# Optimization experiments

Measured on AMD Instinct MI355X. Metric: run time of the kernel, lower is better.

## Reference

```python
import jax, jax.numpy as jnp
import numpy as np

B = 8192
I = 1024  # input_size
H = 1024  # hidden_size


def setup_inputs() -> dict:
    key = jax.random.key(0)
    ks = jax.random.split(key, 8)
    s_i = 1.0 / np.sqrt(I)
    s_h = 1.0 / np.sqrt(H)
    return {
        "x": jax.random.normal(ks[0], (B, I), dtype=jnp.float32),
        "h": jax.random.normal(ks[1], (B, H), dtype=jnp.float32),
        # nn.Linear weights have shape [out, in]; y = x @ W.T
        "W_wz": jax.random.uniform(ks[2], (H, I), jnp.float32, -s_i, s_i),
        "W_uz": jax.random.uniform(ks[3], (H, H), jnp.float32, -s_h, s_h),
        "W_wr": jax.random.uniform(ks[4], (H, I), jnp.float32, -s_i, s_i),
        "W_ur": jax.random.uniform(ks[5], (H, H), jnp.float32, -s_h, s_h),
        "W_u": jax.random.uniform(ks[6], (H, H), jnp.float32, -s_h, s_h),
        "W_w": jax.random.uniform(ks[7], (H, I), jnp.float32, -s_i, s_i),
    }


def reference(x, h, W_wz, W_uz, W_wr, W_ur, W_u, W_w):
    # Fuse the three x-projections and the two h-projections into grouped GEMMs.
    # [B, 3H] = x @ [I, 3H]
    xp = x @ jnp.concatenate([W_wz, W_wr, W_w], axis=0).T
    hp = h @ jnp.concatenate([W_uz, W_ur], axis=0).T  # [B, 2H]
    z = jax.nn.sigmoid(xp[:, :H] + hp[:, :H])
    r = jax.nn.sigmoid(xp[:, H:2 * H] + hp[:, H:])
    h_t = jnp.tanh((r * h) @ W_u.T + xp[:, 2 * H:])
    return z * h + (1.0 - z) * h_t
```

## Files before the change

kernel.cpp:

```cpp
#include <hip/hip_runtime.h>

typedef unsigned short u16;
typedef __attribute__((ext_vector_type(8))) short bf16x8;
typedef __attribute__((ext_vector_type(4))) float f32x4;

__device__ __forceinline__ u16 f2b(float f) {
  unsigned u = __float_as_uint(f);
  u += 0x7FFFu + ((u >> 16) & 1u);
  return (u16)(u >> 16);
}
__device__ __forceinline__ float sigm(float x) { return 1.0f / (1.0f + __expf(-x)); }
__device__ __forceinline__ float tanh_f(float x) { return 1.0f - 2.0f / (__expf(2.0f * x) + 1.0f); }

__device__ __forceinline__ void cp16(const u16* g, u16* l) {
  __builtin_amdgcn_global_load_lds(
      (const __attribute__((address_space(1))) unsigned int*)g,
      (__attribute__((address_space(3))) unsigned int*)l, 16, 0, 0);
}

__global__ __launch_bounds__(256) void pack_xh(const float* __restrict__ x,
                                               const float* __restrict__ h,
                                               u16* __restrict__ xhb) {
  int idx = blockIdx.x * 256 + threadIdx.x;
  int row = idx >> 9;
  int k = (idx & 511) << 2;
  const float* src = (k < 1024) ? (x + row * 1024 + k) : (h + row * 1024 + (k - 1024));
  float4 v = *reinterpret_cast<const float4*>(src);
  ushort4 o = make_ushort4(f2b(v.x), f2b(v.y), f2b(v.z), f2b(v.w));
  *reinterpret_cast<ushort4*>(xhb + ((size_t)idx << 2)) = o;
}

__global__ __launch_bounds__(256) void pack_w1(const float* __restrict__ Wwz,
                                               const float* __restrict__ Wuz,
                                               const float* __restrict__ Wwr,
                                               const float* __restrict__ Wur,
                                               const float* __restrict__ Ww,
                                               u16* __restrict__ W1b) {
  int idx = blockIdx.x * 256 + threadIdx.x;
  int n = idx >> 9;
  int k = (idx & 511) << 2;
  float4 v = make_float4(0.f, 0.f, 0.f, 0.f);
  if (n < 1024) {
    v = (k < 1024) ? *reinterpret_cast<const float4*>(Wwz + n * 1024 + k)
                   : *reinterpret_cast<const float4*>(Wuz + n * 1024 + (k - 1024));
  } else if (n < 2048) {
    int nn = n - 1024;
    v = (k < 1024) ? *reinterpret_cast<const float4*>(Wwr + nn * 1024 + k)
                   : *reinterpret_cast<const float4*>(Wur + nn * 1024 + (k - 1024));
  } else {
    int nn = n - 2048;
    if (k < 1024) v = *reinterpret_cast<const float4*>(Ww + nn * 1024 + k);
  }
  ushort4 o = make_ushort4(f2b(v.x), f2b(v.y), f2b(v.z), f2b(v.w));
  *reinterpret_cast<ushort4*>(W1b + ((size_t)idx << 2)) = o;
}

__global__ __launch_bounds__(256) void pack_wu(const float* __restrict__ Wu,
                                               u16* __restrict__ Wub) {
  int idx = blockIdx.x * 256 + threadIdx.x;
  float4 v = *reinterpret_cast<const float4*>(Wu + ((size_t)idx << 2));
  ushort4 o = make_ushort4(f2b(v.x), f2b(v.y), f2b(v.z), f2b(v.w));
  *reinterpret_cast<ushort4*>(Wub + ((size_t)idx << 2)) = o;
}

__device__ __forceinline__ void gemm_core(const u16* __restrict__ A, const u16* __restrict__ Bm,
                                          int lda, int ldb, int m0, int n0, int ksteps,
                                          u16* a_lds, u16* b_lds, f32x4 acc[4][4]) {
  const int tid = threadIdx.x;
  const int lane = tid & 63;
  const int wave = tid >> 6;
  const int wr = wave >> 1, wc = wave & 1;
  const int srow = tid >> 2;
  const int scol = (tid & 3) << 3;
  const u16* ga = A + (size_t)(m0 + srow) * lda + scol;
  const u16* gb = Bm + (size_t)(n0 + srow) * ldb + scol;
  u16* la = a_lds + tid * 8;
  u16* lb = b_lds + tid * 8;
  const int fr = lane & 15;
  const int fk = (lane >> 4) << 3;

  for (int kt = 0; kt < ksteps; ++kt) {
    const int k0 = kt * 32;
    cp16(ga + k0, la);
    cp16(ga + (size_t)64 * lda + k0, la + 64 * 32);
    cp16(gb + k0, lb);
    cp16(gb + (size_t)64 * ldb + k0, lb + 64 * 32);
    __syncthreads();

    bf16x8 af[4], bfr[4];
#pragma unroll
    for (int m = 0; m < 4; ++m)
      af[m] = *reinterpret_cast<const bf16x8*>(&a_lds[(wr * 64 + m * 16 + fr) * 32 + fk]);
#pragma unroll
    for (int n = 0; n < 4; ++n)
      bfr[n] = *reinterpret_cast<const bf16x8*>(&b_lds[(wc * 64 + n * 16 + fr) * 32 + fk]);
#pragma unroll
    for (int m = 0; m < 4; ++m)
#pragma unroll
      for (int n = 0; n < 4; ++n)
        acc[m][n] = __builtin_amdgcn_mfma_f32_16x16x32_bf16(af[m], bfr[n], acc[m][n], 0, 0, 0);
    __syncthreads();
  }
}

__global__ __launch_bounds__(256) void gemm1_k(const u16* __restrict__ xhb,
                                               const u16* __restrict__ W1b,
                                               const float* __restrict__ h,
                                               float* __restrict__ zout,
                                               u16* __restrict__ rhb,
                                               float* __restrict__ xwb) {
  __shared__ u16 a_lds[128 * 32];
  __shared__ u16 b_lds[128 * 32];
  const int m0 = blockIdx.y * 128;
  const int n0 = blockIdx.x * 128;
  const int ksteps = (n0 >= 2048) ? 32 : 64;
  f32x4 acc[4][4];
#pragma unroll
  for (int m = 0; m < 4; ++m)
#pragma unroll
    for (int n = 0; n < 4; ++n) acc[m][n] = (f32x4){0.f, 0.f, 0.f, 0.f};

  gemm_core(xhb, W1b, 2048, 2048, m0, n0, ksteps, a_lds, b_lds, acc);

  const int lane = threadIdx.x & 63;
  const int wave = threadIdx.x >> 6;
  const int wr = wave >> 1, wc = wave & 1;
  const int rbase = m0 + wr * 64 + ((lane >> 4) << 2);
  const int cbase = n0 + wc * 64 + (lane & 15);
  const int region = n0 >> 10;
#pragma unroll
  for (int m = 0; m < 4; ++m) {
#pragma unroll
    for (int n = 0; n < 4; ++n) {
      const int col = cbase + n * 16;
#pragma unroll
      for (int j = 0; j < 4; ++j) {
        const int row = rbase + m * 16 + j;
        const float v = acc[m][n][j];
        if (region == 0) {
          zout[(size_t)row * 1024 + col] = sigm(v);
        } else if (region == 1) {
          const size_t idx = (size_t)row * 1024 + (col - 1024);
          rhb[idx] = f2b(sigm(v) * h[idx]);
        } else {
          xwb[(size_t)row * 1024 + (col - 2048)] = v;
        }
      }
    }
  }
}

__global__ __launch_bounds__(256) void gemm2_k(const u16* __restrict__ rhb,
                                               const u16* __restrict__ Wub,
                                               const float* __restrict__ h,
                                               const float* __restrict__ xwb,
                                               float* __restrict__ out) {
  __shared__ u16 a_lds[128 * 32];
  __shared__ u16 b_lds[128 * 32];
  const int m0 = blockIdx.y * 128;
  const int n0 = blockIdx.x * 128;
  f32x4 acc[4][4];
#pragma unroll
  for (int m = 0; m < 4; ++m)
#pragma unroll
    for (int n = 0; n < 4; ++n) acc[m][n] = (f32x4){0.f, 0.f, 0.f, 0.f};

  gemm_core(rhb, Wub, 1024, 1024, m0, n0, 32, a_lds, b_lds, acc);

  const int lane = threadIdx.x & 63;
  const int wave = threadIdx.x >> 6;
  const int wr = wave >> 1, wc = wave & 1;
  const int rbase = m0 + wr * 64 + ((lane >> 4) << 2);
  const int cbase = n0 + wc * 64 + (lane & 15);
#pragma unroll
  for (int m = 0; m < 4; ++m) {
#pragma unroll
    for (int n = 0; n < 4; ++n) {
      const int col = cbase + n * 16;
#pragma unroll
      for (int j = 0; j < 4; ++j) {
        const int row = rbase + m * 16 + j;
        const size_t idx = (size_t)row * 1024 + col;
        const float z = out[idx];
        const float hv = h[idx];
        const float ht = tanh_f(acc[m][n][j] + xwb[idx]);
        out[idx] = z * hv + (1.0f - z) * ht;
      }
    }
  }
}

extern "C" void kernel_launch(void* const* d_in, const int* in_sizes, int n_in,
                              void* d_out, int out_size, void* d_ws, size_t ws_size,
                              hipStream_t stream) {
  const float* x   = (const float*)d_in[0];
  const float* h   = (const float*)d_in[1];
  const float* Wwz = (const float*)d_in[2];
  const float* Wuz = (const float*)d_in[3];
  const float* Wwr = (const float*)d_in[4];
  const float* Wur = (const float*)d_in[5];
  const float* Wu  = (const float*)d_in[6];
  const float* Ww  = (const float*)d_in[7];
  float* out = (float*)d_out;

  char* ws = (char*)d_ws;
  u16*   xhb = (u16*)(ws);
  u16*   W1b = (u16*)(ws + 33554432);
  u16*   Wub = (u16*)(ws + 46137344);
  u16*   rhb = (u16*)(ws + 48234496);
  float* xwb = (float*)(ws + 65011712);

  pack_xh<<<16384, 256, 0, stream>>>(x, h, xhb);
  pack_w1<<<6144, 256, 0, stream>>>(Wwz, Wuz, Wwr, Wur, Ww, W1b);
  pack_wu<<<1024, 256, 0, stream>>>(Wu, Wub);
  gemm1_k<<<dim3(24, 64), 256, 0, stream>>>(xhb, W1b, h, out, rhb, xwb);
  gemm2_k<<<dim3(8, 64), 256, 0, stream>>>(rhb, Wub, h, xwb, out);
}
```

Measured before the change: 340.9 us.

## Rewrite GEMM core with 256x256 tiles, double-buffered async LDS and swizzle

Replaces the 128x128 single-buffered GEMM core with a 256x256 tile, 8-wave kernel that uses a K-tile of 64, double-buffered LDS filled by direct global-to-LDS loads, and an XOR swizzle to avoid bank conflicts. Prefetch of the next A tile and the tile after next for B is interleaved with MFMA quarters, using explicit waitcnt, barriers and priority hints. The aim is to hide global load latency, cut per-k-step barrier overhead and raise data reuse per block. In exchange it uses more registers and LDS per block and launches fewer blocks, 384 for the first GEMM and 128 for the second, which may leave CUs underused on the second GEMM.

```diff
diff --git a/kernel.cpp b/kernel.cpp
--- a/kernel.cpp
+++ b/kernel.cpp
@@ -63,80 +63,121 @@
   *reinterpret_cast<ushort4*>(Wub + ((size_t)idx << 2)) = o;
 }
 
-__device__ __forceinline__ void gemm_core(const u16* __restrict__ A, const u16* __restrict__ Bm,
-                                          int lda, int ldb, int m0, int n0, int ksteps,
-                                          u16* a_lds, u16* b_lds, f32x4 acc[4][4]) {
+__device__ __forceinline__ void core8(const u16* __restrict__ Ag, const u16* __restrict__ Bg,
+                                      int lda, int ldb, int NT,
+                                      u16* a_lds, u16* b_lds, f32x4 acc[8][4]) {
   const int tid = threadIdx.x;
   const int lane = tid & 63;
-  const int wave = tid >> 6;
-  const int wr = wave >> 1, wc = wave & 1;
-  const int srow = tid >> 2;
-  const int scol = (tid & 3) << 3;
-  const u16* ga = A + (size_t)(m0 + srow) * lda + scol;
-  const u16* gb = Bm + (size_t)(n0 + srow) * ldb + scol;
-  u16* la = a_lds + tid * 8;
-  u16* lb = b_lds + tid * 8;
-  const int fr = lane & 15;
-  const int fk = (lane >> 4) << 3;
-
-  for (int kt = 0; kt < ksteps; ++kt) {
-    const int k0 = kt * 32;
-    cp16(ga + k0, la);
-    cp16(ga + (size_t)64 * lda + k0, la + 64 * 32);
-    cp16(gb + k0, lb);
-    cp16(gb + (size_t)64 * ldb + k0, lb + 64 * 32);
-    __syncthreads();
-
-    bf16x8 af[4], bfr[4];
-#pragma unroll
-    for (int m = 0; m < 4; ++m)
-      af[m] = *reinterpret_cast<const bf16x8*>(&a_lds[(wr * 64 + m * 16 + fr) * 32 + fk]);
-#pragma unroll
-    for (int n = 0; n < 4; ++n)
-      bfr[n] = *reinterpret_cast<const bf16x8*>(&b_lds[(wc * 64 + n * 16 + fr) * 32 + fk]);
-#pragma unroll
-    for (int m = 0; m < 4; ++m)
-#pragma unroll
-      for (int n = 0; n < 4; ++n)
-        acc[m][n] = __builtin_amdgcn_mfma_f32_16x16x32_bf16(af[m], bfr[n], acc[m][n], 0, 0, 0);
-    __syncthreads();
-  }
-}
-
-__global__ __launch_bounds__(256) void gemm1_k(const u16* __restrict__ xhb,
-                                               const u16* __restrict__ W1b,
-                                               const float* __restrict__ h,
-                                               float* __restrict__ zout,
-                                               u16* __restrict__ rhb,
-                                               float* __restrict__ xwb) {
-  __shared__ u16 a_lds[128 * 32];
-  __shared__ u16 b_lds[128 * 32];
-  const int m0 = blockIdx.y * 128;
-  const int n0 = blockIdx.x * 128;
-  const int ksteps = (n0 >= 2048) ? 32 : 64;
-  f32x4 acc[4][4];
-#pragma unroll
-  for (int m = 0; m < 4; ++m)
+  const int wid = tid >> 6;
+  const int wr = wid >> 2;
+  const int wc = wid & 3;
+
+  const int plo = tid * 16;
+  const int olo = plo ^ (((plo >> 9) & 1) << 5);
+  const int r0 = olo >> 7;
+  const int c2 = olo & 127;
+
+  const int arl = (((lane & 15) * 128) + (((lane >> 4) * 16) ^ (((lane >> 2) & 1) << 5))) >> 1;
+
+  auto stageA = [&](int h, int tg, int tb) {
+    const u16* g = Ag + (size_t)(h * 128 + r0) * lda + (c2 >> 1) + (size_t)tg * 64;
+    u16* l = a_lds + tb * 16384 + h * 8192 + tid * 8;
+    cp16(g, l);
+    cp16(g + (size_t)64 * lda, l + 4096);
+  };
+  auto stageB = [&](int h, int tg, int tb) {
+    const u16* g = Bg + (size_t)(h * 128 + r0) * ldb + (c2 >> 1) + (size_t)tg * 64;
+    u16* l = b_lds + tb * 16384 + h * 8192 + tid * 8;
+    cp16(g, l);
+    cp16(g + (size_t)64 * ldb, l + 4096);
+  };
+
+  stageA(0, 0, 0); stageA(1, 0, 0);
+  stageB(0, 0, 0); stageB(1, 0, 0);
+  stageB(0, 1, 1); stageB(1, 1, 1);
+  asm volatile("s_waitcnt vmcnt(4)" ::: "memory");
+  __builtin_amdgcn_s_barrier();
+  __builtin_amdgcn_sched_barrier(0);
+
+  for (int t = 0; t < NT; ++t) {
+    const int buf = t & 1;
+    const int abase = buf * 16384 + wr * 8192;
+    const int bbase = buf * 16384 + (wc >> 1) * 8192 + (wc & 1) * 4096;
+    bf16x8 bfr[4][2];
+#pragma unroll
+    for (int q = 0; q < 4; ++q) {
+      bf16x8 af[2][2];
+#pragma unroll
+      for (int m = 0; m < 2; ++m)
+#pragma unroll
+        for (int ks = 0; ks < 2; ++ks)
+          af[m][ks] = *reinterpret_cast<const bf16x8*>(
+              a_lds + abase + (q * 2 + m) * 1024 + ks * 32 + arl);
+      if (q == 0) {
+#pragma unroll
+        for (int nf = 0; nf < 4; ++nf)
+#pragma unroll
+          for (int ks = 0; ks < 2; ++ks)
+            bfr[nf][ks] = *reinterpret_cast<const bf16x8*>(
+                b_lds + bbase + nf * 1024 + ks * 32 + arl);
+      }
+      if (q == 0)      { if (t + 1 < NT) stageA(0, t + 1, (t + 1) & 1); }
+      else if (q == 1) { if (t + 1 < NT) stageA(1, t + 1, (t + 1) & 1); }
+      else if (q == 2) { if (t + 2 < NT) stageB(0, t + 2, buf); }
+      else             { if (t + 2 < NT) stageB(1, t + 2, buf);
+                         asm volatile("s_waitcnt vmcnt(4)" ::: "memory"); }
+      __builtin_amdgcn_s_barrier();
+      __builtin_amdgcn_sched_barrier(0);
+      __builtin_amdgcn_s_setprio(1);
+#pragma unroll
+      for (int m = 0; m < 2; ++m)
+#pragma unroll
+        for (int nf = 0; nf < 4; ++nf)
+#pragma unroll
+          for (int ks = 0; ks < 2; ++ks)
+            acc[q * 2 + m][nf] = __builtin_amdgcn_mfma_f32_16x16x32_bf16(
+                af[m][ks], bfr[nf][ks], acc[q * 2 + m][nf], 0, 0, 0);
+      __builtin_amdgcn_s_setprio(0);
+      __builtin_amdgcn_s_barrier();
+      __builtin_amdgcn_sched_barrier(0);
+    }
+  }
+}
+
+__global__ __launch_bounds__(512, 2) void gemm1_k(const u16* __restrict__ xhb,
+                                                  const u16* __restrict__ W1b,
+                                                  const float* __restrict__ h,
+                                                  float* __restrict__ zout,
+                                                  u16* __restrict__ rhb,
+                                                  float* __restrict__ xwb) {
+  __shared__ u16 a_lds[32768];
+  __shared__ u16 b_lds[32768];
+  const int m0 = blockIdx.y * 256;
+  const int n0 = blockIdx.x * 256;
+  const int NT = (n0 >= 2048) ? 16 : 32;
+  f32x4 acc[8][4];
+#pragma unroll
+  for (int m = 0; m < 8; ++m)
 #pragma unroll
     for (int n = 0; n < 4; ++n) acc[m][n] = (f32x4){0.f, 0.f, 0.f, 0.f};
 
-  gemm_core(xhb, W1b, 2048, 2048, m0, n0, ksteps, a_lds, b_lds, acc);
+  core8(xhb + (size_t)m0 * 2048, W1b + (size_t)n0 * 2048, 2048, 2048, NT, a_lds, b_lds, acc);
 
   const int lane = threadIdx.x & 63;
-  const int wave = threadIdx.x >> 6;
-  const int wr = wave >> 1, wc = wave & 1;
-  const int rbase = m0 + wr * 64 + ((lane >> 4) << 2);
+  const int wid = threadIdx.x >> 6;
+  const int wr = wid >> 2, wc = wid & 3;
+  const int rbase = m0 + wr * 128 + ((lane >> 4) << 2);
   const int cbase = n0 + wc * 64 + (lane & 15);
   const int region = n0 >> 10;
 #pragma unroll
-  for (int m = 0; m < 4; ++m) {
-#pragma unroll
-    for (int n = 0; n < 4; ++n) {
-      const int col = cbase + n * 16;
+  for (int mq = 0; mq < 8; ++mq) {
+#pragma unroll
+    for (int nf = 0; nf < 4; ++nf) {
+      const int col = cbase + nf * 16;
 #pragma unroll
       for (int j = 0; j < 4; ++j) {
-        const int row = rbase + m * 16 + j;
-        const float v = acc[m][n][j];
+        const int row = rbase + mq * 16 + j;
+        const float v = acc[mq][nf][j];
         if (region == 0) {
           zout[(size_t)row * 1024 + col] = sigm(v);
         } else if (region == 1) {
@@ -150,40 +191,40 @@
   }
 }
 
-__global__ __launch_bounds__(256) void gemm2_k(const u16* __restrict__ rhb,
-                                               const u16* __restrict__ Wub,
-                                               const float* __restrict__ h,
-                                               const float* __restrict__ xwb,
-                                               float* __restrict__ out) {
-  __shared__ u16 a_lds[128 * 32];
-  __shared__ u16 b_lds[128 * 32];
-  const int m0 = blockIdx.y * 128;
-  const int n0 = blockIdx.x * 128;
-  f32x4 acc[4][4];
-#pragma unroll
-  for (int m = 0; m < 4; ++m)
+__global__ __launch_bounds__(512, 2) void gemm2_k(const u16* __restrict__ rhb,
+                                                  const u16* __restrict__ Wub,
+                                                  const float* __restrict__ h,
+                                                  const float* __restrict__ xwb,
+                                                  float* __restrict__ out) {
+  __shared__ u16 a_lds[32768];
+  __shared__ u16 b_lds[32768];
+  const int m0 = blockIdx.y * 256;
+  const int n0 = blockIdx.x * 256;
+  f32x4 acc[8][4];
+#pragma unroll
+  for (int m = 0; m < 8; ++m)
 #pragma unroll
     for (int n = 0; n < 4; ++n) acc[m][n] = (f32x4){0.f, 0.f, 0.f, 0.f};
 
-  gemm_core(rhb, Wub, 1024, 1024, m0, n0, 32, a_lds, b_lds, acc);
+  core8(rhb + (size_t)m0 * 1024, Wub + (size_t)n0 * 1024, 1024, 1024, 16, a_lds, b_lds, acc);
 
   const int lane = threadIdx.x & 63;
-  const int wave = threadIdx.x >> 6;
-  const int wr = wave >> 1, wc = wave & 1;
-  const int rbase = m0 + wr * 64 + ((lane >> 4) << 2);
+  const int wid = threadIdx.x >> 6;
+  const int wr = wid >> 2, wc = wid & 3;
+  const int rbase = m0 + wr * 128 + ((lane >> 4) << 2);
   const int cbase = n0 + wc * 64 + (lane & 15);
 #pragma unroll
-  for (int m = 0; m < 4; ++m) {
-#pragma unroll
-    for (int n = 0; n < 4; ++n) {
-      const int col = cbase + n * 16;
+  for (int mq = 0; mq < 8; ++mq) {
+#pragma unroll
+    for (int nf = 0; nf < 4; ++nf) {
+      const int col = cbase + nf * 16;
 #pragma unroll
       for (int j = 0; j < 4; ++j) {
-        const int row = rbase + m * 16 + j;
+        const int row = rbase + mq * 16 + j;
         const size_t idx = (size_t)row * 1024 + col;
         const float z = out[idx];
         const float hv = h[idx];
-        const float ht = tanh_f(acc[m][n][j] + xwb[idx]);
+        const float ht = tanh_f(acc[mq][nf][j] + xwb[idx]);
         out[idx] = z * hv + (1.0f - z) * ht;
       }
     }
@@ -213,6 +254,6 @@
   pack_xh<<<16384, 256, 0, stream>>>(x, h, xhb);
   pack_w1<<<6144, 256, 0, stream>>>(Wwz, Wuz, Wwr, Wur, Ww, W1b);
   pack_wu<<<1024, 256, 0, stream>>>(Wu, Wub);
-  gemm1_k<<<dim3(24, 64), 256, 0, stream>>>(xhb, W1b, h, out, rhb, xwb);
-  gemm2_k<<<dim3(8, 64), 256, 0, stream>>>(rhb, Wub, h, xwb, out);
-}
+  gemm1_k<<<dim3(12, 32), 512, 0, stream>>>(xhb, W1b, h, out, rhb, xwb);
+  gemm2_k<<<dim3(4, 32), 512, 0, stream>>>(rhb, Wub, h, xwb, out);
+}
```

After: 387.7 us. +13.7%, slower.
